# Performance work log

Measured on AMD Instinct MI355X. Metric: run time of the kernel, lower is better.

## Reference

```python
import jax, jax.numpy as jnp
import numpy as np

N_HEADS = 16
D_MODEL = 1024
D_HEAD = D_MODEL // N_HEADS


def setup_inputs() -> dict:
    key = jax.random.key(0)
    ks = jax.random.split(key, 5)
    scale = 0.02
    x = jax.random.normal(ks[0], (2, 2048, D_MODEL), dtype=jnp.float32)
    # torch.nn.Linear weights: (out_features, in_features)
    w_in = jax.random.normal(ks[1], (3 * D_MODEL, D_MODEL), dtype=jnp.float32) * scale
    b_in = jax.random.normal(ks[2], (3 * D_MODEL,), dtype=jnp.float32) * scale
    w_out = jax.random.normal(ks[3], (D_MODEL, D_MODEL), dtype=jnp.float32) * scale
    b_out = jax.random.normal(ks[4], (D_MODEL,), dtype=jnp.float32) * scale
    return {"x": x, "w_in": w_in, "b_in": b_in, "w_out": w_out, "b_out": b_out}


def reference(x, w_in, b_in, w_out, b_out):
    B, S, D = x.shape
    H, Dh = N_HEADS, D_HEAD
    qkv = x @ w_in.T + b_in                      # [B,S,3D]
    q, k, v = jnp.split(qkv, 3, axis=-1)
    q = q.reshape(B, S, H, Dh).transpose(0, 2, 1, 3)  # [B,H,S,Dh]
    k = k.reshape(B, S, H, Dh).transpose(0, 2, 1, 3)
    v = v.reshape(B, S, H, Dh).transpose(0, 2, 1, 3)
    scores = jnp.einsum('bhqd,bhkd->bhqk', q, k) / jnp.sqrt(jnp.float32(Dh))
    weights = jax.nn.softmax(scores, axis=-1)
    out = jnp.einsum('bhqk,bhkd->bhqd', weights, v)   # [B,H,S,Dh]
    # Faithful to original: reshape WITHOUT transposing heads back
    out = out.reshape(B, S, D)
    return out @ w_out.T + b_out
```

## Files before the change

kernel.cpp:

```cpp
#include <hip/hip_runtime.h>
#include <math.h>

constexpr int D_MODEL = 1024;
constexpr int N_HEADS = 16;
constexpr int D_HEAD  = 64;
constexpr int SEQ     = 2048;
constexpr int BATCH   = 2;
constexpr int M_ROWS  = BATCH * SEQ;
constexpr int QKV_N   = 3 * D_MODEL;
constexpr int KDIM    = 1024;
constexpr int NROWS   = BATCH * N_HEADS * SEQ;

typedef __bf16 bf16x8 __attribute__((ext_vector_type(8)));
typedef float  f32x4  __attribute__((ext_vector_type(4)));
typedef float  f32x16 __attribute__((ext_vector_type(16)));
typedef unsigned uint2v __attribute__((ext_vector_type(2)));

union U4 { uint4 u; bf16x8 b; ushort s[8]; };
union U2 { uint2 u; ushort s[4]; };

__device__ __forceinline__ unsigned pk2bf(float lo, float hi) {
    union { unsigned u; __bf16 b[2]; } cv;
    cv.b[0] = (__bf16)lo; cv.b[1] = (__bf16)hi;
    return cv.u;
}
__device__ __forceinline__ ushort f2bf(float f) {
    union { ushort s[2]; __bf16 b[2]; } cv;
    cv.b[0] = (__bf16)f;
    return cv.s[0];
}

__device__ __forceinline__ int swz(int row, int bytecol) {
    return row * 128 + (bytecol ^ ((row & 7) << 4));
}

__device__ __forceinline__ void gload16(const void* g, void* l) {
    __builtin_amdgcn_global_load_lds(
        (const __attribute__((address_space(1))) unsigned int*)g,
        (__attribute__((address_space(3))) unsigned int*)l, 16, 0, 0);
}

#define QSCALE 0.18033688011112042f

__global__ __launch_bounds__(256)
void convert3_kernel(const float* __restrict__ x,  ushort* __restrict__ xo,
                     const float* __restrict__ wi, ushort* __restrict__ wio,
                     const float* __restrict__ wo, ushort* __restrict__ woo) {
    const int na = M_ROWS * D_MODEL;
    const int nb = QKV_N * D_MODEL;
    const int nc = D_MODEL * D_MODEL;
    const int total = (na + nb + nc) / 8;
    for (int g = blockIdx.x * blockDim.x + threadIdx.x; g < total;
         g += gridDim.x * blockDim.x) {
        const int i = g * 8;
        const float* src; ushort* dst; int off;
        if (i < na)           { src = x;  dst = xo;  off = i; }
        else if (i < na + nb) { src = wi; dst = wio; off = i - na; }
        else                  { src = wo; dst = woo; off = i - na - nb; }
        const float4 a = *reinterpret_cast<const float4*>(src + off);
        const float4 b = *reinterpret_cast<const float4*>(src + off + 4);
        uint4 o;
        o.x = pk2bf(a.x, a.y); o.y = pk2bf(a.z, a.w);
        o.z = pk2bf(b.x, b.y); o.w = pk2bf(b.z, b.w);
        *reinterpret_cast<uint4*>(dst + off) = o;
    }
}

__device__ __forceinline__ void mfma_gemm_bt_128(
    const ushort* __restrict__ Ag, const ushort* __restrict__ Bg,
    int m0, int n0, ushort* As, ushort* Bs, f32x4 (&acc)[4][4])
{
    const int tid = threadIdx.x;
    const int l   = tid & 63;
    const int rl  = l & 15, hh = l >> 4;
    const int w   = tid >> 6;
    const int wm  = (w >> 1) * 64, wn = (w & 1) * 64;

    const int r0 = tid >> 2;
    const int ce = (tid & 3) * 8;
    const ushort* gA0 = Ag + (size_t)(m0 + r0) * KDIM + ce;
    const ushort* gA1 = gA0 + (size_t)64 * KDIM;
    const ushort* gB0 = Bg + (size_t)(n0 + r0) * KDIM + ce;
    const ushort* gB1 = gB0 + (size_t)64 * KDIM;
    char* lA = (char*)As + tid * 16;
    char* lB = (char*)Bs + tid * 16;

    for (int k0 = 0; k0 < KDIM; k0 += 32) {
        __syncthreads();
        gload16(gA0 + k0, lA);
        gload16(gA1 + k0, lA + 4096);
        gload16(gB0 + k0, lB);
        gload16(gB1 + k0, lB + 4096);
        __syncthreads();

        bf16x8 af[4], bf_[4];
        #pragma unroll
        for (int f = 0; f < 4; ++f)
            af[f]  = *(const bf16x8*)((const char*)As + (wm + f * 16 + rl) * 64 + hh * 16);
        #pragma unroll
        for (int f = 0; f < 4; ++f)
            bf_[f] = *(const bf16x8*)((const char*)Bs + (wn + f * 16 + rl) * 64 + hh * 16);
        #pragma unroll
        for (int i = 0; i < 4; ++i)
            #pragma unroll
            for (int j = 0; j < 4; ++j)
                acc[i][j] = __builtin_amdgcn_mfma_f32_16x16x32_bf16(af[i], bf_[j], acc[i][j], 0, 0, 0);
    }
}

__global__ __launch_bounds__(256)
void qkv_mfma_kernel(const ushort* __restrict__ xb, const ushort* __restrict__ wb,
                     const float* __restrict__ b_in,
                     ushort* __restrict__ Q, ushort* __restrict__ K, ushort* __restrict__ V) {
    __shared__ __align__(16) ushort As[128 * 32];
    __shared__ __align__(16) ushort Bs[128 * 32];

    f32x4 acc[4][4];
    #pragma unroll
    for (int i = 0; i < 4; ++i)
        #pragma unroll
        for (int j = 0; j < 4; ++j) acc[i][j] = (f32x4){0.f, 0.f, 0.f, 0.f};

    const int m0 = blockIdx.y * 128, n0 = blockIdx.x * 128;
    mfma_gemm_bt_128(xb, wb, m0, n0, As, Bs, acc);

    const int l  = threadIdx.x & 63, w = threadIdx.x >> 6;
    const int rl = l & 15, hh = l >> 4;
    const int mb = m0 + (w >> 1) * 64, nb = n0 + (w & 1) * 64;

    #pragma unroll
    for (int j = 0; j < 4; ++j) {
        const int n  = nb + j * 16 + rl;
        const float bias = b_in[n];
        const int t  = n >> 10;
        const int jj = n & 1023;
        const int h  = jj >> 6;
        const int d  = jj & 63;
        ushort* dst = (t == 0) ? Q : (t == 1) ? K : V;
        const float sc = (t == 0) ? QSCALE : 1.0f;
        #pragma unroll
        for (int i = 0; i < 4; ++i)
            #pragma unroll
            for (int r = 0; r < 4; ++r) {
                const int m = mb + i * 16 + hh * 4 + r;
                const int b = m >> 11;
                const int s = m & (SEQ - 1);
                dst[((size_t)(b * N_HEADS + h) * SEQ + s) * D_HEAD + d] =
                    f2bf((acc[i][j][r] + bias) * sc);
            }
    }
}

__global__ __launch_bounds__(512)
void attn_mfma_split_kernel(const ushort* __restrict__ Q, const ushort* __restrict__ K,
                            const ushort* __restrict__ V, ushort* __restrict__ Op,
                            float* __restrict__ lbuf) {
    __shared__ __align__(16) char Ks[2][64 * 128];
    __shared__ __align__(16) char Vs[2][64 * 128];

    const int tid = threadIdx.x;
    const int w   = tid >> 6;
    const int l   = tid & 63;
    const int l31 = l & 31;
    const int lh  = l >> 5;

    const int bid  = blockIdx.x;
    const int nid  = (bid & 7) * 64 + (bid >> 3);
    const int bh   = nid >> 4;
    const int rem  = nid & 15;
    const int half = rem >> 3;
    const int qt   = rem & 7;

    const size_t base  = (size_t)bh * SEQ * D_HEAD;
    const size_t kbase = base + (size_t)half * 1024 * D_HEAD;
    const int qbase = qt * 256 + w * 32;

    bf16x8 qf[4];
    {
        const ushort* qp = Q + base + (size_t)(qbase + l31) * D_HEAD + lh * 8;
        #pragma unroll
        for (int c = 0; c < 4; ++c) {
            U4 t; t.u = *(const uint4*)(qp + c * 16);
            qf[c] = t.b;
        }
    }

    f32x16 ot0, ot1;
    #pragma unroll
    for (int r = 0; r < 16; ++r) { ot0[r] = 0.f; ot1[r] = 0.f; }
    float l_run = 0.0f;

    const int sr  = tid >> 3, seg = tid & 7;
    const int kp  = (tid & 31) * 2, dc = (tid >> 5) * 4;
    const ushort* gK  = K + kbase + (size_t)sr * D_HEAD + seg * 8;
    const ushort* gV0 = V + kbase + (size_t)kp * D_HEAD + dc;
    const ushort* gV1 = gV0 + D_HEAD;

    uint4 ka; U2 va, vb;
    ka   = *(const uint4*)(gK);
    va.u = *(const uint2*)(gV0);
    vb.u = *(const uint2*)(gV1);
    {
        char* kd = Ks[0]; char* vd = Vs[0];
        *(uint4*)(kd + swz(sr, seg * 16)) = ka;
        #pragma unroll
        for (int i = 0; i < 4; ++i) {
            const int d = dc + i;
            *(unsigned*)(vd + d * 128 + ((kp * 2) ^ ((d & 7) << 4))) =
                (unsigned)va.s[i] | ((unsigned)vb.s[i] << 16);
        }
    }

    constexpr int NT = 1024 / 64;
    for (int t = 0; t < NT; ++t) {
        const int cur = t & 1;
        __syncthreads();

        if (t + 1 < NT) {
            const size_t off = (size_t)(t + 1) * 64 * D_HEAD;
            ka   = *(const uint4*)(gK + off);
            va.u = *(const uint2*)(gV0 + off);
            vb.u = *(const uint2*)(gV1 + off);
        }
        const char* kbuf = Ks[cur];
        const char* vbuf = Vs[cur];

        f32x16 st0, st1;
        #pragma unroll
        for (int r = 0; r < 16; ++r) { st0[r] = 0.f; st1[r] = 0.f; }
        #pragma unroll
        for (int c = 0; c < 4; ++c) {
            const bf16x8 kf0 = *(const bf16x8*)(kbuf + swz(l31,      c * 32 + lh * 16));
            st0 = __builtin_amdgcn_mfma_f32_32x32x16_bf16(kf0, qf[c], st0, 0, 0, 0);
            const bf16x8 kf1 = *(const bf16x8*)(kbuf + swz(32 + l31, c * 32 + lh * 16));
            st1 = __builtin_amdgcn_mfma_f32_32x32x16_bf16(kf1, qf[c], st1, 0, 0, 0);
        }

        float ps = 0.f;
        #pragma unroll
        for (int r = 0; r < 16; ++r) {
            st0[r] = __builtin_amdgcn_exp2f(st0[r]); ps += st0[r];
            st1[r] = __builtin_amdgcn_exp2f(st1[r]); ps += st1[r];
        }
        l_run += ps;

        bf16x8 paf[4];
        #pragma unroll
        for (int t32 = 0; t32 < 2; ++t32) {
            const f32x16& s = t32 ? st1 : st0;
            const unsigned q0 = pk2bf(s[0],  s[1]);
            const unsigned q1 = pk2bf(s[2],  s[3]);
            const unsigned q2 = pk2bf(s[4],  s[5]);
            const unsigned q3 = pk2bf(s[6],  s[7]);
            const unsigned q4 = pk2bf(s[8],  s[9]);
            const unsigned q5 = pk2bf(s[10], s[11]);
            const unsigned q6 = pk2bf(s[12], s[13]);
            const unsigned q7 = pk2bf(s[14], s[15]);
            const uint2v x = __builtin_amdgcn_permlane32_swap(q0, q2, false, false);
            const uint2v y = __builtin_amdgcn_permlane32_swap(q1, q3, false, false);
            const uint2v z = __builtin_amdgcn_permlane32_swap(q4, q6, false, false);
            const uint2v u = __builtin_amdgcn_permlane32_swap(q5, q7, false, false);
            U4 f0; f0.u.x = x[0]; f0.u.y = y[0]; f0.u.z = x[1]; f0.u.w = y[1];
            U4 f1; f1.u.x = z[0]; f1.u.y = u[0]; f1.u.z = z[1]; f1.u.w = u[1];
            paf[t32 * 2]     = f0.b;
            paf[t32 * 2 + 1] = f1.b;
        }

        #pragma unroll
        for (int kc = 0; kc < 4; ++kc) {
            const bf16x8 vf0 = *(const bf16x8*)(vbuf + swz(l31,      kc * 32 + lh * 16));
            ot0 = __builtin_amdgcn_mfma_f32_32x32x16_bf16(vf0, paf[kc], ot0, 0, 0, 0);
            const bf16x8 vf1 = *(const bf16x8*)(vbuf + swz(32 + l31, kc * 32 + lh * 16));
            ot1 = __builtin_amdgcn_mfma_f32_32x32x16_bf16(vf1, paf[kc], ot1, 0, 0, 0);
        }

        if (t + 1 < NT) {
            char* kd = Ks[cur ^ 1]; char* vd = Vs[cur ^ 1];
            *(uint4*)(kd + swz(sr, seg * 16)) = ka;
            #pragma unroll
            for (int i = 0; i < 4; ++i) {
                const int d = dc + i;
                *(unsigned*)(vd + d * 128 + ((kp * 2) ^ ((d & 7) << 4))) =
                    (unsigned)va.s[i] | ((unsigned)vb.s[i] << 16);
            }
        }
    }

    l_run += __shfl_xor(l_run, 32, 64);
    const size_t grow = (size_t)bh * SEQ + qbase + l31;
    ushort* op = Op + ((size_t)half * NROWS + grow) * D_HEAD;
    #pragma unroll
    for (int dt = 0; dt < 2; ++dt) {
        const f32x16& o = dt ? ot1 : ot0;
        #pragma unroll
        for (int g = 0; g < 4; ++g) {
            const int d0 = dt * 32 + g * 8 + lh * 4;
            uint2 s2;
            s2.x = pk2bf(o[g * 4 + 0], o[g * 4 + 1]);
            s2.y = pk2bf(o[g * 4 + 2], o[g * 4 + 3]);
            *(uint2*)(op + d0) = s2;
        }
    }
    if (lh == 0) lbuf[(size_t)half * NROWS + grow] = l_run;
}

__global__ __launch_bounds__(256)
void combine_kernel(const ushort* __restrict__ Op, const float* __restrict__ lbuf,
                    ushort* __restrict__ A) {
    const int idx = blockIdx.x * 256 + threadIdx.x;
    const int row = idx >> 3;
    const int dc  = (idx & 7) * 8;
    const float inv = 1.0f / (lbuf[row] + lbuf[NROWS + row]);
    U4 o1, o2;
    o1.u = *(const uint4*)(Op + (size_t)row * D_HEAD + dc);
    o2.u = *(const uint4*)(Op + ((size_t)NROWS + row) * D_HEAD + dc);
    uint4 r;
    float v[8];
    #pragma unroll
    for (int i = 0; i < 8; ++i)
        v[i] = ((float)o1.b[i] + (float)o2.b[i]) * inv;
    r.x = pk2bf(v[0], v[1]); r.y = pk2bf(v[2], v[3]);
    r.z = pk2bf(v[4], v[5]); r.w = pk2bf(v[6], v[7]);
    *(uint4*)(A + (size_t)row * D_HEAD + dc) = r;
}

__global__ __launch_bounds__(256)
void out_mfma_kernel(const ushort* __restrict__ Ab, const ushort* __restrict__ wb,
                     const float* __restrict__ b_out, float* __restrict__ out) {
    __shared__ __align__(16) ushort As[128 * 32];
    __shared__ __align__(16) ushort Bs[128 * 32];

    f32x4 acc[4][4];
    #pragma unroll
    for (int i = 0; i < 4; ++i)
        #pragma unroll
        for (int j = 0; j < 4; ++j) acc[i][j] = (f32x4){0.f, 0.f, 0.f, 0.f};

    const int m0 = blockIdx.y * 128, n0 = blockIdx.x * 128;
    mfma_gemm_bt_128(Ab, wb, m0, n0, As, Bs, acc);

    const int l  = threadIdx.x & 63, w = threadIdx.x >> 6;
    const int rl = l & 15, hh = l >> 4;
    const int mb = m0 + (w >> 1) * 64, nb = n0 + (w & 1) * 64;

    #pragma unroll
    for (int j = 0; j < 4; ++j) {
        const int n = nb + j * 16 + rl;
        const float bias = b_out[n];
        #pragma unroll
        for (int i = 0; i < 4; ++i)
            #pragma unroll
            for (int r = 0; r < 4; ++r) {
                const int m = mb + i * 16 + hh * 4 + r;
                out[(size_t)m * D_MODEL + n] = acc[i][j][r] + bias;
            }
    }
}

extern "C" void kernel_launch(void* const* d_in, const int* in_sizes, int n_in,
                              void* d_out, int out_size, void* d_ws, size_t ws_size,
                              hipStream_t stream) {
    const float* x     = (const float*)d_in[0];
    const float* w_in  = (const float*)d_in[1];
    const float* b_in  = (const float*)d_in[2];
    const float* w_out = (const float*)d_in[3];
    const float* b_out = (const float*)d_in[4];
    float* out = (float*)d_out;

    const size_t T = (size_t)BATCH * N_HEADS * SEQ * D_HEAD;
    ushort* Qw  = (ushort*)d_ws;
    ushort* Kw  = Qw + T;
    ushort* Vw  = Kw + T;
    ushort* Opw = Vw + T;
    ushort* xb  = Opw + T;
    ushort* wib = xb + T;
    ushort* wob = wib + (size_t)QKV_N * D_MODEL;
    float*  lw  = (float*)(wob + (size_t)D_MODEL * D_MODEL);
    ushort* Aw  = Qw;

    convert3_kernel<<<2048, 256, 0, stream>>>(x, xb, w_in, wib, w_out, wob);

    qkv_mfma_kernel<<<dim3(QKV_N / 128, M_ROWS / 128), 256, 0, stream>>>(
        xb, wib, b_in, Qw, Kw, Vw);
    attn_mfma_split_kernel<<<512, 512, 0, stream>>>(Qw, Kw, Vw, Opw, lw);
    combine_kernel<<<NROWS * 8 / 256, 256, 0, stream>>>(Opw, lw, Aw);
    out_mfma_kernel<<<dim3(D_MODEL / 128, M_ROWS / 128), 256, 0, stream>>>(
        Aw, wob, b_out, out);
}
```

Before: 125.3 us.

## Process two 64-key sub-tiles per barrier in split attention loop

The attention kernel now stages 128 keys per iteration as two 64-key sub-tiles in double-buffered shared memory, halving the number of loop iterations and __syncthreads barriers. Global prefetch loads are issued for both sub-tiles at once to increase memory-level parallelism. The exp-sum reduction is split into four independent accumulators to shorten the dependency chain. In exchange, LDS use doubles to 64KB per block and register pressure rises, which may reduce occupancy.

```diff
diff --git a/kernel.cpp b/kernel.cpp
--- a/kernel.cpp
+++ b/kernel.cpp
@@ -41,6 +41,24 @@
 }
 
 #define QSCALE 0.18033688011112042f
+
+__device__ __forceinline__ void pack_paf(const f32x16& s, bf16x8& f0o, bf16x8& f1o) {
+    const unsigned q0 = pk2bf(s[0],  s[1]);
+    const unsigned q1 = pk2bf(s[2],  s[3]);
+    const unsigned q2 = pk2bf(s[4],  s[5]);
+    const unsigned q3 = pk2bf(s[6],  s[7]);
+    const unsigned q4 = pk2bf(s[8],  s[9]);
+    const unsigned q5 = pk2bf(s[10], s[11]);
+    const unsigned q6 = pk2bf(s[12], s[13]);
+    const unsigned q7 = pk2bf(s[14], s[15]);
+    const uint2v x = __builtin_amdgcn_permlane32_swap(q0, q2, false, false);
+    const uint2v y = __builtin_amdgcn_permlane32_swap(q1, q3, false, false);
+    const uint2v z = __builtin_amdgcn_permlane32_swap(q4, q6, false, false);
+    const uint2v u = __builtin_amdgcn_permlane32_swap(q5, q7, false, false);
+    U4 f0; f0.u.x = x[0]; f0.u.y = y[0]; f0.u.z = x[1]; f0.u.w = y[1];
+    U4 f1; f1.u.x = z[0]; f1.u.y = u[0]; f1.u.z = z[1]; f1.u.w = u[1];
+    f0o = f0.b; f1o = f1.b;
+}
 
 __global__ __launch_bounds__(256)
 void convert3_kernel(const float* __restrict__ x,  ushort* __restrict__ xo,
@@ -155,8 +173,8 @@
 void attn_mfma_split_kernel(const ushort* __restrict__ Q, const ushort* __restrict__ K,
                             const ushort* __restrict__ V, ushort* __restrict__ Op,
                             float* __restrict__ lbuf) {
-    __shared__ __align__(16) char Ks[2][64 * 128];
-    __shared__ __align__(16) char Vs[2][64 * 128];
+    __shared__ __align__(16) char Ks[2][2][64 * 128];
+    __shared__ __align__(16) char Vs[2][2][64 * 128];
 
     const int tid = threadIdx.x;
     const int w   = tid >> 6;
@@ -196,92 +214,92 @@
     const ushort* gV0 = V + kbase + (size_t)kp * D_HEAD + dc;
     const ushort* gV1 = gV0 + D_HEAD;
 
-    uint4 ka; U2 va, vb;
-    ka   = *(const uint4*)(gK);
-    va.u = *(const uint2*)(gV0);
-    vb.u = *(const uint2*)(gV1);
-    {
-        char* kd = Ks[0]; char* vd = Vs[0];
-        *(uint4*)(kd + swz(sr, seg * 16)) = ka;
+    uint4 ka[2]; U2 va[2], vb[2];
+    #pragma unroll
+    for (int s = 0; s < 2; ++s) {
+        const size_t so = (size_t)s * 64 * D_HEAD;
+        ka[s].x = 0;
+        ka[s]   = *(const uint4*)(gK + so);
+        va[s].u = *(const uint2*)(gV0 + so);
+        vb[s].u = *(const uint2*)(gV1 + so);
+    }
+    #pragma unroll
+    for (int s = 0; s < 2; ++s) {
+        char* kd = Ks[0][s]; char* vd = Vs[0][s];
+        *(uint4*)(kd + swz(sr, seg * 16)) = ka[s];
         #pragma unroll
         for (int i = 0; i < 4; ++i) {
             const int d = dc + i;
             *(unsigned*)(vd + d * 128 + ((kp * 2) ^ ((d & 7) << 4))) =
-                (unsigned)va.s[i] | ((unsigned)vb.s[i] << 16);
-        }
-    }
-
-    constexpr int NT = 1024 / 64;
+                (unsigned)va[s].s[i] | ((unsigned)vb[s].s[i] << 16);
+        }
+    }
+
+    constexpr int NT = 1024 / 128;
     for (int t = 0; t < NT; ++t) {
         const int cur = t & 1;
         __syncthreads();
 
         if (t + 1 < NT) {
-            const size_t off = (size_t)(t + 1) * 64 * D_HEAD;
-            ka   = *(const uint4*)(gK + off);
-            va.u = *(const uint2*)(gV0 + off);
-            vb.u = *(const uint2*)(gV1 + off);
-        }
-        const char* kbuf = Ks[cur];
-        const char* vbuf = Vs[cur];
-
-        f32x16 st0, st1;
-        #pragma unroll
-        for (int r = 0; r < 16; ++r) { st0[r] = 0.f; st1[r] = 0.f; }
-        #pragma unroll
-        for (int c = 0; c < 4; ++c) {
-            const bf16x8 kf0 = *(const bf16x8*)(kbuf + swz(l31,      c * 32 + lh * 16));
-            st0 = __builtin_amdgcn_mfma_f32_32x32x16_bf16(kf0, qf[c], st0, 0, 0, 0);
-            const bf16x8 kf1 = *(const bf16x8*)(kbuf + swz(32 + l31, c * 32 + lh * 16));
-            st1 = __builtin_amdgcn_mfma_f32_32x32x16_bf16(kf1, qf[c], st1, 0, 0, 0);
-        }
-
-        float ps = 0.f;
-        #pragma unroll
-        for (int r = 0; r < 16; ++r) {
-            st0[r] = __builtin_amdgcn_exp2f(st0[r]); ps += st0[r];
-            st1[r] = __builtin_amdgcn_exp2f(st1[r]); ps += st1[r];
-        }
-        l_run += ps;
-
-        bf16x8 paf[4];
-        #pragma unroll
-        for (int t32 = 0; t32 < 2; ++t32) {
-            const f32x16& s = t32 ? st1 : st0;
-            const unsigned q0 = pk2bf(s[0],  s[1]);
-            const unsigned q1 = pk2bf(s[2],  s[3]);
-            const unsigned q2 = pk2bf(s[4],  s[5]);
-            const unsigned q3 = pk2bf(s[6],  s[7]);
-            const unsigned q4 = pk2bf(s[8],  s[9]);
-            const unsigned q5 = pk2bf(s[10], s[11]);
-            const unsigned q6 = pk2bf(s[12], s[13]);
-            const unsigned q7 = pk2bf(s[14], s[15]);
-            const uint2v x = __builtin_amdgcn_permlane32_swap(q0, q2, false, false);
-            const uint2v y = __builtin_amdgcn_permlane32_swap(q1, q3, false, false);
-            const uint2v z = __builtin_amdgcn_permlane32_swap(q4, q6, false, false);
-            const uint2v u = __builtin_amdgcn_permlane32_swap(q5, q7, false, false);
-            U4 f0; f0.u.x = x[0]; f0.u.y = y[0]; f0.u.z = x[1]; f0.u.w = y[1];
-            U4 f1; f1.u.x = z[0]; f1.u.y = u[0]; f1.u.z = z[1]; f1.u.w = u[1];
-            paf[t32 * 2]     = f0.b;
-            paf[t32 * 2 + 1] = f1.b;
-        }
-
-        #pragma unroll
-        for (int kc = 0; kc < 4; ++kc) {
-            const bf16x8 vf0 = *(const bf16x8*)(vbuf + swz(l31,      kc * 32 + lh * 16));
-            ot0 = __builtin_amdgcn_mfma_f32_32x32x16_bf16(vf0, paf[kc], ot0, 0, 0, 0);
-            const bf16x8 vf1 = *(const bf16x8*)(vbuf + swz(32 + l31, kc * 32 + lh * 16));
-            ot1 = __builtin_amdgcn_mfma_f32_32x32x16_bf16(vf1, paf[kc], ot1, 0, 0, 0);
+            #pragma unroll
+            for (int s = 0; s < 2; ++s) {
+                const size_t off = ((size_t)(t + 1) * 128 + s * 64) * D_HEAD;
+                ka[s]   = *(const uint4*)(gK + off);
+                va[s].u = *(const uint2*)(gV0 + off);
+                vb[s].u = *(const uint2*)(gV1 + off);
+            }
+        }
+
+        #pragma unroll
+        for (int s = 0; s < 2; ++s) {
+            const char* kbuf = Ks[cur][s];
+            const char* vbuf = Vs[cur][s];
+
+            f32x16 st0, st1;
+            #pragma unroll
+            for (int r = 0; r < 16; ++r) { st0[r] = 0.f; st1[r] = 0.f; }
+            #pragma unroll
+            for (int c = 0; c < 4; ++c) {
+                const bf16x8 kf0 = *(const bf16x8*)(kbuf + swz(l31,      c * 32 + lh * 16));
+                st0 = __builtin_amdgcn_mfma_f32_32x32x16_bf16(kf0, qf[c], st0, 0, 0, 0);
+                const bf16x8 kf1 = *(const bf16x8*)(kbuf + swz(32 + l31, c * 32 + lh * 16));
+                st1 = __builtin_amdgcn_mfma_f32_32x32x16_bf16(kf1, qf[c], st1, 0, 0, 0);
+            }
+
+            float pa = 0.f, pb = 0.f, pc = 0.f, pd = 0.f;
+            #pragma unroll
+            for (int r = 0; r < 8; ++r) {
+                st0[r]     = __builtin_amdgcn_exp2f(st0[r]);     pa += st0[r];
+                st0[8 + r] = __builtin_amdgcn_exp2f(st0[8 + r]); pb += st0[8 + r];
+                st1[r]     = __builtin_amdgcn_exp2f(st1[r]);     pc += st1[r];
+                st1[8 + r] = __builtin_amdgcn_exp2f(st1[8 + r]); pd += st1[8 + r];
+            }
+            l_run += (pa + pb) + (pc + pd);
+
+            bf16x8 paf[4];
+            pack_paf(st0, paf[0], paf[1]);
+            pack_paf(st1, paf[2], paf[3]);
+
+            #pragma unroll
+            for (int kc = 0; kc < 4; ++kc) {
+                const bf16x8 vf0 = *(const bf16x8*)(vbuf + swz(l31,      kc * 32 + lh * 16));
+                ot0 = __builtin_amdgcn_mfma_f32_32x32x16_bf16(vf0, paf[kc], ot0, 0, 0, 0);
+                const bf16x8 vf1 = *(const bf16x8*)(vbuf + swz(32 + l31, kc * 32 + lh * 16));
+                ot1 = __builtin_amdgcn_mfma_f32_32x32x16_bf16(vf1, paf[kc], ot1, 0, 0, 0);
+            }
         }
 
         if (t + 1 < NT) {
-            char* kd = Ks[cur ^ 1]; char* vd = Vs[cur ^ 1];
-            *(uint4*)(kd + swz(sr, seg * 16)) = ka;
-            #pragma unroll
-            for (int i = 0; i < 4; ++i) {
-                const int d = dc + i;
-                *(unsigned*)(vd + d * 128 + ((kp * 2) ^ ((d & 7) << 4))) =
-                    (unsigned)va.s[i] | ((unsigned)vb.s[i] << 16);
+            #pragma unroll
+            for (int s = 0; s < 2; ++s) {
+                char* kd = Ks[cur ^ 1][s]; char* vd = Vs[cur ^ 1][s];
+                *(uint4*)(kd + swz(sr, seg * 16)) = ka[s];
+                #pragma unroll
+                for (int i = 0; i < 4; ++i) {
+                    const int d = dc + i;
+                    *(unsigned*)(vd + d * 128 + ((kp * 2) ^ ((d & 7) << 4))) =
+                        (unsigned)va[s].s[i] | ((unsigned)vb[s].s[i] << 16);
+                }
             }
         }
     }
```

Measured after the change: 128.0 us. 1.02x slower.

## Double-buffer LDS in GEMM tiles and split softmax row-sum accumulation

Applied to the files above, without the earlier changes.

The shared GEMM helper used by the QKV and output projections now keeps two LDS stages. It prefetches the next K-slab via global_load_lds while MFMAs run on the current slab, which cuts one barrier per iteration and hides global load latency. The attention softmax sum is split into four independent accumulators to shorten the dependent add chain, and the P-packing code moves into a helper function. Doubling LDS per block may reduce occupancy, and the single remaining barrier relies on the async LDS loads completing before it.

```diff
diff --git a/kernel.cpp b/kernel.cpp
--- a/kernel.cpp
+++ b/kernel.cpp
@@ -41,6 +41,24 @@
 }
 
 #define QSCALE 0.18033688011112042f
+
+__device__ __forceinline__ void pack_paf(const f32x16& s, bf16x8& f0o, bf16x8& f1o) {
+    const unsigned q0 = pk2bf(s[0],  s[1]);
+    const unsigned q1 = pk2bf(s[2],  s[3]);
+    const unsigned q2 = pk2bf(s[4],  s[5]);
+    const unsigned q3 = pk2bf(s[6],  s[7]);
+    const unsigned q4 = pk2bf(s[8],  s[9]);
+    const unsigned q5 = pk2bf(s[10], s[11]);
+    const unsigned q6 = pk2bf(s[12], s[13]);
+    const unsigned q7 = pk2bf(s[14], s[15]);
+    const uint2v x = __builtin_amdgcn_permlane32_swap(q0, q2, false, false);
+    const uint2v y = __builtin_amdgcn_permlane32_swap(q1, q3, false, false);
+    const uint2v z = __builtin_amdgcn_permlane32_swap(q4, q6, false, false);
+    const uint2v u = __builtin_amdgcn_permlane32_swap(q5, q7, false, false);
+    U4 f0; f0.u.x = x[0]; f0.u.y = y[0]; f0.u.z = x[1]; f0.u.w = y[1];
+    U4 f1; f1.u.x = z[0]; f1.u.y = u[0]; f1.u.z = z[1]; f1.u.w = u[1];
+    f0o = f0.b; f1o = f1.b;
+}
 
 __global__ __launch_bounds__(256)
 void convert3_kernel(const float* __restrict__ x,  ushort* __restrict__ xo,
@@ -66,9 +84,10 @@
     }
 }
 
-__device__ __forceinline__ void mfma_gemm_bt_128(
+__device__ __forceinline__ void mfma_gemm_bt_128_2ph(
     const ushort* __restrict__ Ag, const ushort* __restrict__ Bg,
-    int m0, int n0, ushort* As, ushort* Bs, f32x4 (&acc)[4][4])
+    int m0, int n0, ushort (*As)[128 * 32], ushort (*Bs)[128 * 32],
+    f32x4 (&acc)[4][4])
 {
     const int tid = threadIdx.x;
     const int l   = tid & 63;
@@ -82,29 +101,36 @@
     const ushort* gA1 = gA0 + (size_t)64 * KDIM;
     const ushort* gB0 = Bg + (size_t)(n0 + r0) * KDIM + ce;
     const ushort* gB1 = gB0 + (size_t)64 * KDIM;
-    char* lA = (char*)As + tid * 16;
-    char* lB = (char*)Bs + tid * 16;
-
+    const int lo = tid * 16;
+
+    gload16(gA0, (char*)As[0] + lo);
+    gload16(gA1, (char*)As[0] + lo + 4096);
+    gload16(gB0, (char*)Bs[0] + lo);
+    gload16(gB1, (char*)Bs[0] + lo + 4096);
+    __syncthreads();
+
+    int cur = 0;
     for (int k0 = 0; k0 < KDIM; k0 += 32) {
-        __syncthreads();
-        gload16(gA0 + k0, lA);
-        gload16(gA1 + k0, lA + 4096);
-        gload16(gB0 + k0, lB);
-        gload16(gB1 + k0, lB + 4096);
-        __syncthreads();
-
+        if (k0 + 32 < KDIM) {
+            gload16(gA0 + k0 + 32, (char*)As[cur ^ 1] + lo);
+            gload16(gA1 + k0 + 32, (char*)As[cur ^ 1] + lo + 4096);
+            gload16(gB0 + k0 + 32, (char*)Bs[cur ^ 1] + lo);
+            gload16(gB1 + k0 + 32, (char*)Bs[cur ^ 1] + lo + 4096);
+        }
         bf16x8 af[4], bf_[4];
         #pragma unroll
         for (int f = 0; f < 4; ++f)
-            af[f]  = *(const bf16x8*)((const char*)As + (wm + f * 16 + rl) * 64 + hh * 16);
+            af[f]  = *(const bf16x8*)((const char*)As[cur] + (wm + f * 16 + rl) * 64 + hh * 16);
         #pragma unroll
         for (int f = 0; f < 4; ++f)
-            bf_[f] = *(const bf16x8*)((const char*)Bs + (wn + f * 16 + rl) * 64 + hh * 16);
+            bf_[f] = *(const bf16x8*)((const char*)Bs[cur] + (wn + f * 16 + rl) * 64 + hh * 16);
         #pragma unroll
         for (int i = 0; i < 4; ++i)
             #pragma unroll
             for (int j = 0; j < 4; ++j)
                 acc[i][j] = __builtin_amdgcn_mfma_f32_16x16x32_bf16(af[i], bf_[j], acc[i][j], 0, 0, 0);
+        __syncthreads();
+        cur ^= 1;
     }
 }
 
@@ -112,8 +138,8 @@
 void qkv_mfma_kernel(const ushort* __restrict__ xb, const ushort* __restrict__ wb,
                      const float* __restrict__ b_in,
                      ushort* __restrict__ Q, ushort* __restrict__ K, ushort* __restrict__ V) {
-    __shared__ __align__(16) ushort As[128 * 32];
-    __shared__ __align__(16) ushort Bs[128 * 32];
+    __shared__ __align__(16) ushort As[2][128 * 32];
+    __shared__ __align__(16) ushort Bs[2][128 * 32];
 
     f32x4 acc[4][4];
     #pragma unroll
@@ -122,7 +148,7 @@
         for (int j = 0; j < 4; ++j) acc[i][j] = (f32x4){0.f, 0.f, 0.f, 0.f};
 
     const int m0 = blockIdx.y * 128, n0 = blockIdx.x * 128;
-    mfma_gemm_bt_128(xb, wb, m0, n0, As, Bs, acc);
+    mfma_gemm_bt_128_2ph(xb, wb, m0, n0, As, Bs, acc);
 
     const int l  = threadIdx.x & 63, w = threadIdx.x >> 6;
     const int rl = l & 15, hh = l >> 4;
@@ -236,35 +262,19 @@
             st1 = __builtin_amdgcn_mfma_f32_32x32x16_bf16(kf1, qf[c], st1, 0, 0, 0);
         }
 
-        float ps = 0.f;
-        #pragma unroll
-        for (int r = 0; r < 16; ++r) {
-            st0[r] = __builtin_amdgcn_exp2f(st0[r]); ps += st0[r];
-            st1[r] = __builtin_amdgcn_exp2f(st1[r]); ps += st1[r];
-        }
-        l_run += ps;
+        float pa = 0.f, pb = 0.f, pc = 0.f, pd = 0.f;
+        #pragma unroll
+        for (int r = 0; r < 8; ++r) {
+            st0[r]     = __builtin_amdgcn_exp2f(st0[r]);     pa += st0[r];
+            st0[8 + r] = __builtin_amdgcn_exp2f(st0[8 + r]); pb += st0[8 + r];
+            st1[r]     = __builtin_amdgcn_exp2f(st1[r]);     pc += st1[r];
+            st1[8 + r] = __builtin_amdgcn_exp2f(st1[8 + r]); pd += st1[8 + r];
+        }
+        l_run += (pa + pb) + (pc + pd);
 
         bf16x8 paf[4];
-        #pragma unroll
-        for (int t32 = 0; t32 < 2; ++t32) {
-            const f32x16& s = t32 ? st1 : st0;
-            const unsigned q0 = pk2bf(s[0],  s[1]);
-            const unsigned q1 = pk2bf(s[2],  s[3]);
-            const unsigned q2 = pk2bf(s[4],  s[5]);
-            const unsigned q3 = pk2bf(s[6],  s[7]);
-            const unsigned q4 = pk2bf(s[8],  s[9]);
-            const unsigned q5 = pk2bf(s[10], s[11]);
-            const unsigned q6 = pk2bf(s[12], s[13]);
-            const unsigned q7 = pk2bf(s[14], s[15]);
-            const uint2v x = __builtin_amdgcn_permlane32_swap(q0, q2, false, false);
-            const uint2v y = __builtin_amdgcn_permlane32_swap(q1, q3, false, false);
-            const uint2v z = __builtin_amdgcn_permlane32_swap(q4, q6, false, false);
-            const uint2v u = __builtin_amdgcn_permlane32_swap(q5, q7, false, false);
-            U4 f0; f0.u.x = x[0]; f0.u.y = y[0]; f0.u.z = x[1]; f0.u.w = y[1];
-            U4 f1; f1.u.x = z[0]; f1.u.y = u[0]; f1.u.z = z[1]; f1.u.w = u[1];
-            paf[t32 * 2]     = f0.b;
-            paf[t32 * 2 + 1] = f1.b;
-        }
+        pack_paf(st0, paf[0], paf[1]);
+        pack_paf(st1, paf[2], paf[3]);
 
         #pragma unroll
         for (int kc = 0; kc < 4; ++kc) {
@@ -327,8 +337,8 @@
 __global__ __launch_bounds__(256)
 void out_mfma_kernel(const ushort* __restrict__ Ab, const ushort* __restrict__ wb,
                      const float* __restrict__ b_out, float* __restrict__ out) {
-    __shared__ __align__(16) ushort As[128 * 32];
-    __shared__ __align__(16) ushort Bs[128 * 32];
+    __shared__ __align__(16) ushort As[2][128 * 32];
+    __shared__ __align__(16) ushort Bs[2][128 * 32];
 
     f32x4 acc[4][4];
     #pragma unroll
@@ -337,7 +347,7 @@
         for (int j = 0; j < 4; ++j) acc[i][j] = (f32x4){0.f, 0.f, 0.f, 0.f};
 
     const int m0 = blockIdx.y * 128, n0 = blockIdx.x * 128;
-    mfma_gemm_bt_128(Ab, wb, m0, n0, As, Bs, acc);
+    mfma_gemm_bt_128_2ph(Ab, wb, m0, n0, As, Bs, acc);
 
     const int l  = threadIdx.x & 63, w = threadIdx.x >> 6;
     const int rl = l & 15, hh = l >> 4;
```

New measurement: 120.1 us, median of 2. 4.2% less time.
